# Kernel tuning notes

Measured on AMD Instinct MI355X. Metric: run time of the kernel, lower is better.

The kernel has to match this reference:

```python
import jax, jax.numpy as jnp
import numpy as np


def setup_inputs() -> dict:
    key = jax.random.key(0)
    ks = jax.random.split(key, 4)
    L, B, T, H, D = 12, 4, 2048, 16, 64
    current_layer = jax.random.normal(ks[0], (B, T, H, D), dtype=jnp.float32)
    all_layers = jax.random.normal(ks[1], (L, B, T, H, D), dtype=jnp.float32)
    # nn.init.normal_(std=0.02) for both projections
    Wq = jax.random.normal(ks[2], (D, D), dtype=jnp.float32) * 0.02
    Wk = jax.random.normal(ks[3], (D, D), dtype=jnp.float32) * 0.02
    scales = jnp.full((L,), 1.0 / L, dtype=jnp.float32)  # LayerScalingFactor init 1/num_layers
    temperature = jnp.ones((1,), dtype=jnp.float32)
    return {
        "current_layer": current_layer,
        "all_layers": all_layers,
        "Wq": Wq,
        "Wk": Wk,
        "scales": scales,
        "temperature": temperature,
        "current_layer_idx": 0,
    }


def reference(current_layer, all_layers, Wq, Wk, scales, temperature, current_layer_idx):
    # current_layer: [B,T,H,D]; all_layers: [L,B,T,H,D] (stack of per-layer outputs)
    # num_heads = 1, so per-head dim == D and scores are over the layer axis L.
    D = current_layer.shape[-1]
    q = jnp.einsum("bthd,ed->bthe", current_layer, Wq)          # query_proj (no bias)
    k = jnp.einsum("lbthd,ed->lbthe", all_layers, Wk)           # key_proj (no bias)
    inv_scale = 1.0 / (jnp.sqrt(jnp.asarray(D, q.dtype)) * jnp.abs(temperature[0]))
    scores = jnp.einsum("bthd,lbthd->bthl", q, k) * inv_scale   # [B,T,H,L]
    attn = jax.nn.softmax(scores, axis=-1)
    attn = attn * scales                                        # per-layer learned scale
    attn = attn / (jnp.sum(attn, axis=-1, keepdims=True) + 1e-6)  # renormalize
    # per-layer accumulation: output += scales[l] * attn[...,l] * all_layers[l]
    out = jnp.einsum("bthl,l,lbthd->bthd", attn, scales, all_layers)
    return out
```

## Files before the change

kernel.cpp:

```cpp
#include <hip/hip_runtime.h>

constexpr int L = 12;
constexpr int B = 4, T = 2048, H = 16, D = 64;
constexpr int NPOS = B * T * H;
constexpr long long SLAYER = (long long)NPOS * D;

__global__ __launch_bounds__(64) void cla_precompute_M(
    const float* __restrict__ Wq, const float* __restrict__ Wk,
    float* __restrict__ M) {
  const int d  = blockIdx.x;
  const int d2 = threadIdx.x;
  float acc = 0.f;
  #pragma unroll
  for (int e = 0; e < D; ++e)
    acc = fmaf(Wq[e * D + d], Wk[e * D + d2], acc);
  M[d * D + d2] = acc;
}

__global__ __launch_bounds__(256) void cla_main(
    const float* __restrict__ cur, const float* __restrict__ all,
    const float* __restrict__ M, const float* __restrict__ scales,
    const float* __restrict__ temperature, float* __restrict__ out) {
  __shared__ float Mlds[D * D];
  {
    const float4* src = (const float4*)M;
    float4* dst = (float4*)Mlds;
    #pragma unroll
    for (int i = 0; i < 4; ++i)
      dst[threadIdx.x + 256 * i] = src[threadIdx.x + 256 * i];
  }
  __syncthreads();

  const int gt = blockIdx.x * 256 + threadIdx.x;
  const int p  = gt >> 4;
  const int j  = gt & 15;

  const float inv_scale = 1.0f / (8.0f * fabsf(temperature[0]));

  float scl[L];
  #pragma unroll
  for (int l = 0; l < L; ++l) scl[l] = scales[l];

  const size_t base = (size_t)p * D + (size_t)j * 4;
  const float4 xv = *(const float4*)(cur + base);

  float4 y[L];
  #pragma unroll
  for (int l = 0; l < L; ++l)
    y[l] = *(const float4*)(all + (size_t)l * SLAYER + base);

  float v0 = 0.f, v1 = 0.f, v2 = 0.f, v3 = 0.f;
  const float xc[4] = {xv.x, xv.y, xv.z, xv.w};
  #pragma unroll
  for (int d = 0; d < D; ++d) {
    const float xd = __shfl(xc[d & 3], d >> 2, 16);
    const float4 m = *(const float4*)(Mlds + d * D + j * 4);
    v0 = fmaf(xd, m.x, v0);
    v1 = fmaf(xd, m.y, v1);
    v2 = fmaf(xd, m.z, v2);
    v3 = fmaf(xd, m.w, v3);
  }

  float sc[L];
  #pragma unroll
  for (int l = 0; l < L; ++l) {
    float s = v0 * y[l].x + v1 * y[l].y + v2 * y[l].z + v3 * y[l].w;
    s += __shfl_xor(s, 1, 16);
    s += __shfl_xor(s, 2, 16);
    s += __shfl_xor(s, 4, 16);
    s += __shfl_xor(s, 8, 16);
    sc[l] = s * inv_scale;
  }

  float mx = sc[0];
  #pragma unroll
  for (int l = 1; l < L; ++l) mx = fmaxf(mx, sc[l]);
  float sum = 0.f;
  #pragma unroll
  for (int l = 0; l < L; ++l) { sc[l] = __expf(sc[l] - mx); sum += sc[l]; }
  const float inv_sum = 1.0f / sum;

  float w[L];
  float ssum = 0.f;
  #pragma unroll
  for (int l = 0; l < L; ++l) { w[l] = sc[l] * inv_sum * scl[l]; ssum += w[l]; }
  const float r = 1.0f / (ssum + 1e-6f);

  float o0 = 0.f, o1 = 0.f, o2 = 0.f, o3 = 0.f;
  #pragma unroll
  for (int l = 0; l < L; ++l) {
    const float wl = w[l] * r * scl[l];
    o0 = fmaf(wl, y[l].x, o0);
    o1 = fmaf(wl, y[l].y, o1);
    o2 = fmaf(wl, y[l].z, o2);
    o3 = fmaf(wl, y[l].w, o3);
  }
  *(float4*)(out + base) = make_float4(o0, o1, o2, o3);
}

extern "C" void kernel_launch(void* const* d_in, const int* in_sizes, int n_in,
                              void* d_out, int out_size, void* d_ws, size_t ws_size,
                              hipStream_t stream) {
  const float* cur    = (const float*)d_in[0];
  const float* all    = (const float*)d_in[1];
  const float* Wq     = (const float*)d_in[2];
  const float* Wk     = (const float*)d_in[3];
  const float* scales = (const float*)d_in[4];
  const float* temp   = (const float*)d_in[5];
  float* M = (float*)d_ws;

  cla_precompute_M<<<64, 64, 0, stream>>>(Wq, Wk, M);

  const int total_threads = NPOS * 16;
  cla_main<<<total_threads / 256, 256, 0, stream>>>(cur, all, M, scales, temp,
                                                    (float*)d_out);
}
```

Baseline: 107.3 us.

## Remap to one position per wave with register-resident M and DPP reductions

Restructures the main kernel so each wave handles 16 consecutive positions, with each lane owning one feature dimension and holding a column of the transposed M in registers instead of LDS. Layer scores are reduced across the whole wave using DPP row operations and readlane rather than 16-lane shuffles. This removes LDS staging, the block barrier and the shuffle-based query projection. In exchange it uses scalar loads, more registers and fewer, longer-running waves, which may reduce memory latency hiding.

```diff
diff --git a/kernel.cpp b/kernel.cpp
--- a/kernel.cpp
+++ b/kernel.cpp
@@ -4,98 +4,126 @@
 constexpr int B = 4, T = 2048, H = 16, D = 64;
 constexpr int NPOS = B * T * H;
 constexpr long long SLAYER = (long long)NPOS * D;
+constexpr int P = 16;
 
-__global__ __launch_bounds__(64) void cla_precompute_M(
+__global__ __launch_bounds__(64) void cla_precompute_Mt(
     const float* __restrict__ Wq, const float* __restrict__ Wk,
-    float* __restrict__ M) {
-  const int d  = blockIdx.x;
-  const int d2 = threadIdx.x;
+    float* __restrict__ Mt) {
+  const int d = blockIdx.x;
+  const int c = threadIdx.x;
   float acc = 0.f;
   #pragma unroll
   for (int e = 0; e < D; ++e)
-    acc = fmaf(Wq[e * D + d], Wk[e * D + d2], acc);
-  M[d * D + d2] = acc;
+    acc = fmaf(Wq[e * D + d], Wk[e * D + c], acc);
+  Mt[c * D + d] = acc;
+}
+
+template <int CTRL, int ROWM>
+__device__ __forceinline__ float dpp_add(float x) {
+  int moved = __builtin_amdgcn_update_dpp(0, __float_as_int(x), CTRL, ROWM, 0xF,
+                                          false);
+  return x + __int_as_float(moved);
+}
+
+__device__ __forceinline__ float wave_sum_bcast(float x) {
+  x = dpp_add<0x111, 0xF>(x);
+  x = dpp_add<0x112, 0xF>(x);
+  x = dpp_add<0x114, 0xF>(x);
+  x = dpp_add<0x118, 0xF>(x);
+  x = dpp_add<0x142, 0xA>(x);
+  x = dpp_add<0x143, 0xC>(x);
+  return __int_as_float(__builtin_amdgcn_readlane(__float_as_int(x), 63));
 }
 
 __global__ __launch_bounds__(256) void cla_main(
     const float* __restrict__ cur, const float* __restrict__ all,
-    const float* __restrict__ M, const float* __restrict__ scales,
+    const float* __restrict__ Mt, const float* __restrict__ scales,
     const float* __restrict__ temperature, float* __restrict__ out) {
-  __shared__ float Mlds[D * D];
+  const int lane = threadIdx.x & 63;
+  const int wloc = __builtin_amdgcn_readfirstlane(threadIdx.x >> 6);
+  const int wid  = blockIdx.x * 4 + wloc;
+
+  float Mc[D];
   {
-    const float4* src = (const float4*)M;
-    float4* dst = (float4*)Mlds;
+    const float4* mt = (const float4*)(Mt + lane * D);
     #pragma unroll
-    for (int i = 0; i < 4; ++i)
-      dst[threadIdx.x + 256 * i] = src[threadIdx.x + 256 * i];
+    for (int c = 0; c < 16; ++c) {
+      const float4 m = mt[c];
+      Mc[4 * c + 0] = m.x;
+      Mc[4 * c + 1] = m.y;
+      Mc[4 * c + 2] = m.z;
+      Mc[4 * c + 3] = m.w;
+    }
   }
-  __syncthreads();
-
-  const int gt = blockIdx.x * 256 + threadIdx.x;
-  const int p  = gt >> 4;
-  const int j  = gt & 15;
 
   const float inv_scale = 1.0f / (8.0f * fabsf(temperature[0]));
-
   float scl[L];
   #pragma unroll
   for (int l = 0; l < L; ++l) scl[l] = scales[l];
 
-  const size_t base = (size_t)p * D + (size_t)j * 4;
-  const float4 xv = *(const float4*)(cur + base);
+  const int pos0 = wid * P;
+  for (int it = 0; it < P; ++it) {
+    const int pos = pos0 + it;
+    const size_t pbase = (size_t)pos * D;
 
-  float4 y[L];
-  #pragma unroll
-  for (int l = 0; l < L; ++l)
-    y[l] = *(const float4*)(all + (size_t)l * SLAYER + base);
+    const float4* xp = (const float4*)(cur + pbase);
+    float v = 0.f;
+    #pragma unroll
+    for (int dc = 0; dc < 4; ++dc) {
+      const float4 a = xp[4 * dc + 0];
+      const float4 b = xp[4 * dc + 1];
+      const float4 c = xp[4 * dc + 2];
+      const float4 d = xp[4 * dc + 3];
+      v = fmaf(a.x, Mc[16 * dc + 0], v);
+      v = fmaf(a.y, Mc[16 * dc + 1], v);
+      v = fmaf(a.z, Mc[16 * dc + 2], v);
+      v = fmaf(a.w, Mc[16 * dc + 3], v);
+      v = fmaf(b.x, Mc[16 * dc + 4], v);
+      v = fmaf(b.y, Mc[16 * dc + 5], v);
+      v = fmaf(b.z, Mc[16 * dc + 6], v);
+      v = fmaf(b.w, Mc[16 * dc + 7], v);
+      v = fmaf(c.x, Mc[16 * dc + 8], v);
+      v = fmaf(c.y, Mc[16 * dc + 9], v);
+      v = fmaf(c.z, Mc[16 * dc + 10], v);
+      v = fmaf(c.w, Mc[16 * dc + 11], v);
+      v = fmaf(d.x, Mc[16 * dc + 12], v);
+      v = fmaf(d.y, Mc[16 * dc + 13], v);
+      v = fmaf(d.z, Mc[16 * dc + 14], v);
+      v = fmaf(d.w, Mc[16 * dc + 15], v);
+    }
 
-  float v0 = 0.f, v1 = 0.f, v2 = 0.f, v3 = 0.f;
-  const float xc[4] = {xv.x, xv.y, xv.z, xv.w};
-  #pragma unroll
-  for (int d = 0; d < D; ++d) {
-    const float xd = __shfl(xc[d & 3], d >> 2, 16);
-    const float4 m = *(const float4*)(Mlds + d * D + j * 4);
-    v0 = fmaf(xd, m.x, v0);
-    v1 = fmaf(xd, m.y, v1);
-    v2 = fmaf(xd, m.z, v2);
-    v3 = fmaf(xd, m.w, v3);
+    float yv[L];
+    #pragma unroll
+    for (int l = 0; l < L; ++l)
+      yv[l] = all[(size_t)l * SLAYER + pbase + lane];
+
+    float sc[L];
+    #pragma unroll
+    for (int l = 0; l < L; ++l)
+      sc[l] = wave_sum_bcast(v * yv[l]) * inv_scale;
+
+    float mx = sc[0];
+    #pragma unroll
+    for (int l = 1; l < L; ++l) mx = fmaxf(mx, sc[l]);
+    float sum = 0.f;
+    #pragma unroll
+    for (int l = 0; l < L; ++l) { sc[l] = __expf(sc[l] - mx); sum += sc[l]; }
+    const float inv_sum = 1.0f / sum;
+
+    float w[L];
+    float ssum = 0.f;
+    #pragma unroll
+    for (int l = 0; l < L; ++l) {
+      w[l] = sc[l] * inv_sum * scl[l];
+      ssum += w[l];
+    }
+    const float r = 1.0f / (ssum + 1e-6f);
+
+    float o = 0.f;
+    #pragma unroll
+    for (int l = 0; l < L; ++l) o = fmaf(w[l] * r * scl[l], yv[l], o);
+    out[pbase + lane] = o;
   }
-
-  float sc[L];
-  #pragma unroll
-  for (int l = 0; l < L; ++l) {
-    float s = v0 * y[l].x + v1 * y[l].y + v2 * y[l].z + v3 * y[l].w;
-    s += __shfl_xor(s, 1, 16);
-    s += __shfl_xor(s, 2, 16);
-    s += __shfl_xor(s, 4, 16);
-    s += __shfl_xor(s, 8, 16);
-    sc[l] = s * inv_scale;
-  }
-
-  float mx = sc[0];
-  #pragma unroll
-  for (int l = 1; l < L; ++l) mx = fmaxf(mx, sc[l]);
-  float sum = 0.f;
-  #pragma unroll
-  for (int l = 0; l < L; ++l) { sc[l] = __expf(sc[l] - mx); sum += sc[l]; }
-  const float inv_sum = 1.0f / sum;
-
-  float w[L];
-  float ssum = 0.f;
-  #pragma unroll
-  for (int l = 0; l < L; ++l) { w[l] = sc[l] * inv_sum * scl[l]; ssum += w[l]; }
-  const float r = 1.0f / (ssum + 1e-6f);
-
-  float o0 = 0.f, o1 = 0.f, o2 = 0.f, o3 = 0.f;
-  #pragma unroll
-  for (int l = 0; l < L; ++l) {
-    const float wl = w[l] * r * scl[l];
-    o0 = fmaf(wl, y[l].x, o0);
-    o1 = fmaf(wl, y[l].y, o1);
-    o2 = fmaf(wl, y[l].z, o2);
-    o3 = fmaf(wl, y[l].w, o3);
-  }
-  *(float4*)(out + base) = make_float4(o0, o1, o2, o3);
 }
 
 extern "C" void kernel_launch(void* const* d_in, const int* in_sizes, int n_in,
@@ -107,11 +135,12 @@
   const float* Wk     = (const float*)d_in[3];
   const float* scales = (const float*)d_in[4];
   const float* temp   = (const float*)d_in[5];
-  float* M = (float*)d_ws;
+  float* Mt = (float*)d_ws;
 
-  cla_precompute_M<<<64, 64, 0, stream>>>(Wq, Wk, M);
+  cla_precompute_Mt<<<64, 64, 0, stream>>>(Wq, Wk, Mt);
 
-  const int total_threads = NPOS * 16;
-  cla_main<<<total_threads / 256, 256, 0, stream>>>(cur, all, M, scales, temp,
-                                                    (float*)d_out);
+  const int nwaves  = NPOS / P;
+  const int nblocks = nwaves / 4;
+  cla_main<<<nblocks, 256, 0, stream>>>(cur, all, Mt, scales, temp,
+                                        (float*)d_out);
 }
```

Result: slower. 121.4 us (+13.2%).
